# Optimization experiments

Measured on AMD Instinct MI355X. Metric: run time of the kernel, lower is better.

The kernel has to match this reference:

```python
import jax, jax.numpy as jnp
import numpy as np

BETA = 0.25

def setup_inputs() -> dict:
    key = jax.random.key(0)
    k1, k2 = jax.random.split(key)
    N, K, D = 262144, 1024, 64
    z = jax.random.normal(k1, (N, D), dtype=jnp.float32)
    codebook = jax.random.normal(k2, (K, D), dtype=jnp.float32)
    return {"z": z, "codebook": codebook}

def reference(z, codebook):
    # Squared Euclidean distances (argmin identical to torch.cdist argmin):
    # ||z||^2 - 2 z.C^T + ||C||^2 , shape [N, K]
    z_sq = jnp.sum(z * z, axis=1, keepdims=True)            # [N,1]
    c_sq = jnp.sum(codebook * codebook, axis=1)             # [K]
    dist = z_sq - 2.0 * (z @ codebook.T) + c_sq[None, :]    # [N,K]
    indices = jnp.argmin(dist, axis=1)                      # [N] int
    z_q = codebook[indices]                                 # [N,D]
    codebook_loss = jnp.mean((jax.lax.stop_gradient(z_q) - z) ** 2)
    commitment_loss = jnp.mean((z_q - jax.lax.stop_gradient(z)) ** 2)
    vq_loss = codebook_loss + BETA * commitment_loss
    z_q_st = z + jax.lax.stop_gradient(z_q - z)             # straight-through
    return (z_q_st, vq_loss, indices, z_q)
```

## Files before the change

kernel.cpp:

```cpp
#include <hip/hip_runtime.h>
#include <hip/hip_bf16.h>

typedef __bf16 bf16x8 __attribute__((ext_vector_type(8)));
typedef float  f32x4  __attribute__((ext_vector_type(4)));

static constexpr int N_ROWS  = 262144;
static constexpr int K_CODES = 1024;
static constexpr int D_DIM   = 64;

static constexpr long LOSS_OFF = (long)N_ROWS * D_DIM;
static constexpr long IDX_OFF  = LOSS_OFF + 1;
static constexpr long ZQ_OFF   = IDX_OFF + N_ROWS;

static constexpr size_t CSQ_B   = 0;
static constexpr size_t BFRAG_B = 4096;
static constexpr size_t CNT_B   = BFRAG_B + (size_t)16 * 16384;
static constexpr size_t PART_B  = CNT_B + 256;
static constexpr size_t LIST_B  = PART_B + (size_t)16384 * 4;
static constexpr size_t WS_NEEDED = LIST_B + (size_t)N_ROWS * 4;

static constexpr float MARGIN = 0.05f;
static constexpr int   EPI_BLOCKS = (N_ROWS * D_DIM) / (256 * 4);
static constexpr int   RESCORE_BLOCKS = 2048;

#define GLOAD_LDS16(g, l) __builtin_amdgcn_global_load_lds( \
    (const __attribute__((address_space(1))) unsigned int*)(g), \
    (__attribute__((address_space(3))) unsigned int*)(l), 16, 0, 0)

__global__ __launch_bounds__(256) void fusedprep_kernel(const float* __restrict__ cb,
                                                        char* __restrict__ wsb) {
    const int t = blockIdx.x * 256 + threadIdx.x;
    if (t == 0) *(int*)(wsb + CNT_B) = 0;

    if (t < K_CODES) {
        const float4* row = reinterpret_cast<const float4*>(cb) + (size_t)t * (D_DIM / 4);
        float s = 0.f;
        #pragma unroll
        for (int j = 0; j < D_DIM / 4; ++j) {
            float4 v = row[j];
            s = fmaf(v.x, v.x, s); s = fmaf(v.y, v.y, s);
            s = fmaf(v.z, v.z, s); s = fmaf(v.w, v.w, s);
        }
        ((float*)(wsb + CSQ_B))[t] = s;
    }

    const int c  = t >> 3;
    const int ks = (t >> 2) & 1;
    const int g  = t & 3;
    const float* src = cb + (size_t)c * 64 + ks * 32 + g * 8;
    float f[8];
    #pragma unroll
    for (int i = 0; i < 8; ++i) f[i] = src[i];
    bf16x8 h, l;
    #pragma unroll
    for (int i = 0; i < 8; ++i) {
        __bf16 hv = (__bf16)f[i];
        h[i] = hv;
        l[i] = (__bf16)(f[i] - (float)hv);
    }
    const int tile = c >> 6, cf = (c >> 4) & 3, n = c & 15;
    const int lane = g * 16 + n;
    char* base = wsb + BFRAG_B + (size_t)tile * 16384;
    *reinterpret_cast<bf16x8*>(base + ((0 * 2 + ks) * 4 + cf) * 1024 + lane * 16) = h;
    *reinterpret_cast<bf16x8*>(base + ((1 * 2 + ks) * 4 + cf) * 1024 + lane * 16) = l;
}

__global__ __launch_bounds__(256, 2) void vq_gemm_kernel(const float* __restrict__ z,
                                                         char* __restrict__ wsb,
                                                         float* __restrict__ out) {
    __shared__ __align__(16) unsigned char sbuf[2 * 16384 + 4096];
    float* lds_csq = (float*)(sbuf + 32768);

    const int tid  = threadIdx.x;
    const int lane = tid & 63, wid = tid >> 6;
    const int l15  = lane & 15, lg = lane >> 4;

    const float* csq = (const float*)(wsb + CSQ_B);
    #pragma unroll
    for (int i = 0; i < 4; ++i) lds_csq[tid + 256 * i] = csq[tid + 256 * i];

    const int rowbase = blockIdx.x * 256 + wid * 64;
    bf16x8 ah[4][2], al[4][2];
    #pragma unroll
    for (int rf = 0; rf < 4; ++rf) {
        const float* zr = z + (size_t)(rowbase + rf * 16 + l15) * 64 + lg * 8;
        #pragma unroll
        for (int ks = 0; ks < 2; ++ks) {
            float4 a = *reinterpret_cast<const float4*>(zr + ks * 32);
            float4 b = *reinterpret_cast<const float4*>(zr + ks * 32 + 4);
            float f[8] = {a.x, a.y, a.z, a.w, b.x, b.y, b.z, b.w};
            bf16x8 h, l;
            #pragma unroll
            for (int i = 0; i < 8; ++i) {
                __bf16 hv = (__bf16)f[i];
                h[i] = hv;
                l[i] = (__bf16)(f[i] - (float)hv);
            }
            ah[rf][ks] = h; al[rf][ks] = l;
        }
    }

    float m1[16], m2[16]; int i1[16];
    #pragma unroll
    for (int s = 0; s < 16; ++s) { m1[s] = INFINITY; m2[s] = INFINITY; i1[s] = 0; }

    const char* bsrc = wsb + BFRAG_B;
    auto stage = [&](int buf, int t) {
        const char* src = bsrc + (size_t)t * 16384;
        #pragma unroll
        for (int it = 0; it < 4; ++it) {
            GLOAD_LDS16(src + it * 4096 + wid * 1024 + lane * 16,
                        sbuf + buf * 16384 + it * 4096 + wid * 1024);
        }
    };

    stage(0, 0);
    __syncthreads();

    for (int t = 0; t < 16; ++t) {
        if (t < 15) stage((t + 1) & 1, t + 1);
        const unsigned char* B = sbuf + (t & 1) * 16384;
        #pragma unroll
        for (int cf = 0; cf < 4; ++cf) {
            bf16x8 bh0 = *reinterpret_cast<const bf16x8*>(B + (0 * 4 + cf) * 1024 + lane * 16);
            bf16x8 bh1 = *reinterpret_cast<const bf16x8*>(B + (1 * 4 + cf) * 1024 + lane * 16);
            bf16x8 bl0 = *reinterpret_cast<const bf16x8*>(B + (2 * 4 + cf) * 1024 + lane * 16);
            bf16x8 bl1 = *reinterpret_cast<const bf16x8*>(B + (3 * 4 + cf) * 1024 + lane * 16);
            const int code = t * 64 + cf * 16 + l15;
            const float cq = lds_csq[code];
            #pragma unroll
            for (int rf = 0; rf < 4; ++rf) {
                f32x4 acc = {0.f, 0.f, 0.f, 0.f};
                acc = __builtin_amdgcn_mfma_f32_16x16x32_bf16(ah[rf][0], bh0, acc, 0, 0, 0);
                acc = __builtin_amdgcn_mfma_f32_16x16x32_bf16(ah[rf][1], bh1, acc, 0, 0, 0);
                acc = __builtin_amdgcn_mfma_f32_16x16x32_bf16(al[rf][0], bh0, acc, 0, 0, 0);
                acc = __builtin_amdgcn_mfma_f32_16x16x32_bf16(al[rf][1], bh1, acc, 0, 0, 0);
                acc = __builtin_amdgcn_mfma_f32_16x16x32_bf16(ah[rf][0], bl0, acc, 0, 0, 0);
                acc = __builtin_amdgcn_mfma_f32_16x16x32_bf16(ah[rf][1], bl1, acc, 0, 0, 0);
                #pragma unroll
                for (int r = 0; r < 4; ++r) {
                    float dist = fmaf(-2.f, acc[r], cq);
                    int s = rf * 4 + r;
                    bool lt = dist < m1[s];
                    m2[s] = fminf(m2[s], fmaxf(dist, m1[s]));
                    m1[s] = fminf(m1[s], dist);
                    i1[s] = lt ? code : i1[s];
                }
            }
        }
        __syncthreads();
    }

    #pragma unroll
    for (int s = 0; s < 16; ++s) {
        #pragma unroll
        for (int off = 1; off < 16; off <<= 1) {
            float om1 = __shfl_xor(m1[s], off);
            float om2 = __shfl_xor(m2[s], off);
            int   oi  = __shfl_xor(i1[s], off);
            bool lt = (om1 < m1[s]) || (om1 == m1[s] && oi < i1[s]);
            m2[s] = fminf(fminf(m2[s], om2), fmaxf(m1[s], om1));
            m1[s] = fminf(m1[s], om1);
            i1[s] = lt ? oi : i1[s];
        }
    }

    if (l15 == 0) {
        int* cnt  = (int*)(wsb + CNT_B);
        int* list = (int*)(wsb + LIST_B);
        #pragma unroll
        for (int rf = 0; rf < 4; ++rf) {
            #pragma unroll
            for (int r = 0; r < 4; ++r) {
                int s = rf * 4 + r;
                int row = rowbase + rf * 16 + lg * 4 + r;
                out[IDX_OFF + row] = (float)i1[s];
                if (m2[s] - m1[s] < MARGIN) {
                    int pos = atomicAdd(cnt, 1);
                    if (pos < N_ROWS) list[pos] = row;
                }
            }
        }
    }
}

__global__ __launch_bounds__(256) void rescore_kernel(const float* __restrict__ z,
                                                      const float* __restrict__ cb,
                                                      const char* __restrict__ wsb,
                                                      float* __restrict__ out) {
    const int lane = threadIdx.x & 63;
    const int wgid = (blockIdx.x * 256 + threadIdx.x) >> 6;
    int cnt = *(const int*)(wsb + CNT_B);
    if (cnt > N_ROWS) cnt = N_ROWS;
    const int*   list = (const int*)(wsb + LIST_B);
    const float* csq  = (const float*)(wsb + CSQ_B);

    for (int i = wgid; i < cnt; i += RESCORE_BLOCKS * 4) {
        const int row = list[i];
        float4 zr[16];
        const float4* zp = reinterpret_cast<const float4*>(z) + (size_t)row * 16;
        #pragma unroll
        for (int j = 0; j < 16; ++j) zr[j] = zp[j];
        float best = INFINITY; int bi = 0;
        for (int k = lane; k < K_CODES; k += 64) {
            const float4* cp = reinterpret_cast<const float4*>(cb) + (size_t)k * 16;
            float d0 = 0.f, d1 = 0.f, d2 = 0.f, d3 = 0.f;
            #pragma unroll
            for (int j = 0; j < 16; j += 4) {
                float4 c0 = cp[j + 0], c1 = cp[j + 1], c2 = cp[j + 2], c3 = cp[j + 3];
                d0 = fmaf(zr[j+0].x, c0.x, fmaf(zr[j+0].y, c0.y, fmaf(zr[j+0].z, c0.z, fmaf(zr[j+0].w, c0.w, d0))));
                d1 = fmaf(zr[j+1].x, c1.x, fmaf(zr[j+1].y, c1.y, fmaf(zr[j+1].z, c1.z, fmaf(zr[j+1].w, c1.w, d1))));
                d2 = fmaf(zr[j+2].x, c2.x, fmaf(zr[j+2].y, c2.y, fmaf(zr[j+2].z, c2.z, fmaf(zr[j+2].w, c2.w, d2))));
                d3 = fmaf(zr[j+3].x, c3.x, fmaf(zr[j+3].y, c3.y, fmaf(zr[j+3].z, c3.z, fmaf(zr[j+3].w, c3.w, d3))));
            }
            float dist = fmaf(-2.f, (d0 + d1) + (d2 + d3), csq[k]);
            if (dist < best) { best = dist; bi = k; }
        }
        #pragma unroll
        for (int off = 1; off < 64; off <<= 1) {
            float ob = __shfl_xor(best, off);
            int   oi = __shfl_xor(bi, off);
            if (ob < best || (ob == best && oi < bi)) { best = ob; bi = oi; }
        }
        if (lane == 0) out[IDX_OFF + row] = (float)bi;
    }
}

__global__ __launch_bounds__(256) void gather_kernel(const float* __restrict__ z,
                                                     const float* __restrict__ cb,
                                                     float* __restrict__ out,
                                                     float* __restrict__ part) {
    const long g4 = (long)blockIdx.x * 256 + threadIdx.x;
    const long g  = g4 * 4;
    const int  r  = (int)(g >> 6);
    const int  d  = (int)(g & 63);
    const int k = (int)out[IDX_OFF + r];
    float4 zv = reinterpret_cast<const float4*>(z)[g4];
    float4 cv = reinterpret_cast<const float4*>(cb)[(long)k * 16 + (d >> 2)];
    float4 st;
    st.x = zv.x + (cv.x - zv.x); st.y = zv.y + (cv.y - zv.y);
    st.z = zv.z + (cv.z - zv.z); st.w = zv.w + (cv.w - zv.w);
    reinterpret_cast<float4*>(out)[g4] = st;
    float* zq = out + ZQ_OFF + g;
    zq[0] = cv.x; zq[1] = cv.y; zq[2] = cv.z; zq[3] = cv.w;
    float dx = cv.x - zv.x, dy = cv.y - zv.y, dz = cv.z - zv.z, dw = cv.w - zv.w;
    float s = fmaf(dx, dx, fmaf(dy, dy, fmaf(dz, dz, dw * dw)));
    #pragma unroll
    for (int off = 32; off > 0; off >>= 1) s += __shfl_down(s, off, 64);
    __shared__ float wsum[4];
    const int lane = threadIdx.x & 63, wid = threadIdx.x >> 6;
    if (lane == 0) wsum[wid] = s;
    __syncthreads();
    if (threadIdx.x == 0)
        part[blockIdx.x] = (wsum[0] + wsum[1]) + (wsum[2] + wsum[3]);
}

__global__ __launch_bounds__(256) void loss_kernel(const float* __restrict__ part,
                                                   float* __restrict__ out) {
    double s = 0.0;
    for (int i = threadIdx.x; i < EPI_BLOCKS; i += 256) s += (double)part[i];
    #pragma unroll
    for (int off = 32; off > 0; off >>= 1) s += __shfl_down(s, off, 64);
    __shared__ double dsum[4];
    const int lane = threadIdx.x & 63, wid = threadIdx.x >> 6;
    if (lane == 0) dsum[wid] = s;
    __syncthreads();
    if (threadIdx.x == 0) {
        double total = (dsum[0] + dsum[1]) + (dsum[2] + dsum[3]);
        out[LOSS_OFF] = (float)(1.25 * (total / (double)((long)N_ROWS * D_DIM)));
    }
}

__global__ __launch_bounds__(256) void csq_kernel(const float* __restrict__ cb,
                                                  float* __restrict__ ws) {
    int g = blockIdx.x * 256 + threadIdx.x;
    const float4* row = reinterpret_cast<const float4*>(cb) + (size_t)g * (D_DIM / 4);
    float s = 0.f;
    #pragma unroll
    for (int j = 0; j < D_DIM / 4; ++j) {
        float4 v = row[j];
        s = fmaf(v.x, v.x, s); s = fmaf(v.y, v.y, s);
        s = fmaf(v.z, v.z, s); s = fmaf(v.w, v.w, s);
    }
    ws[g] = s;
}

__global__ __launch_bounds__(256) void argmin_old_kernel(const float* __restrict__ z,
                                                         const float* __restrict__ cb,
                                                         const float* __restrict__ ws,
                                                         float* __restrict__ out) {
    __shared__ float4 tile[64 * 16];
    __shared__ float  csq_sh[64];
    const int row = blockIdx.x * 256 + threadIdx.x;
    float4 zr[16];
    const float4* zp = reinterpret_cast<const float4*>(z) + (size_t)row * 16;
    #pragma unroll
    for (int j = 0; j < 16; ++j) zr[j] = zp[j];
    float best = __builtin_inff();
    int   bidx = 0;
    for (int k0 = 0; k0 < K_CODES; k0 += 64) {
        __syncthreads();
        const float4* src = reinterpret_cast<const float4*>(cb) + (size_t)k0 * 16;
        #pragma unroll
        for (int j = 0; j < 4; ++j)
            tile[threadIdx.x + 256 * j] = src[threadIdx.x + 256 * j];
        if (threadIdx.x < 64) csq_sh[threadIdx.x] = ws[k0 + threadIdx.x];
        __syncthreads();
        #pragma unroll 2
        for (int k = 0; k < 64; ++k) {
            float d0 = 0.f, d1 = 0.f, d2 = 0.f, d3 = 0.f;
            #pragma unroll
            for (int j = 0; j < 16; j += 4) {
                float4 c0 = tile[k*16+j+0], c1 = tile[k*16+j+1], c2 = tile[k*16+j+2], c3 = tile[k*16+j+3];
                d0 = fmaf(zr[j+0].x, c0.x, fmaf(zr[j+0].y, c0.y, fmaf(zr[j+0].z, c0.z, fmaf(zr[j+0].w, c0.w, d0))));
                d1 = fmaf(zr[j+1].x, c1.x, fmaf(zr[j+1].y, c1.y, fmaf(zr[j+1].z, c1.z, fmaf(zr[j+1].w, c1.w, d1))));
                d2 = fmaf(zr[j+2].x, c2.x, fmaf(zr[j+2].y, c2.y, fmaf(zr[j+2].z, c2.z, fmaf(zr[j+2].w, c2.w, d2))));
                d3 = fmaf(zr[j+3].x, c3.x, fmaf(zr[j+3].y, c3.y, fmaf(zr[j+3].z, c3.z, fmaf(zr[j+3].w, c3.w, d3))));
            }
            float dist = fmaf(-2.f, (d0 + d1) + (d2 + d3), csq_sh[k]);
            if (dist < best) { best = dist; bidx = k0 + k; }
        }
    }
    out[IDX_OFF + row] = (float)bidx;
}

extern "C" void kernel_launch(void* const* d_in, const int* in_sizes, int n_in,
                              void* d_out, int out_size, void* d_ws, size_t ws_size,
                              hipStream_t stream) {
    (void)in_sizes; (void)n_in; (void)out_size;
    const float* z  = (const float*)d_in[0];
    const float* cb = (const float*)d_in[1];
    float* out = (float*)d_out;
    char*  wsb = (char*)d_ws;
    float* wsf = (float*)d_ws;

    if (ws_size >= WS_NEEDED) {
        fusedprep_kernel<<<32,             256, 0, stream>>>(cb, wsb);
        vq_gemm_kernel  <<<N_ROWS / 256,   256, 0, stream>>>(z, wsb, out);
        rescore_kernel  <<<RESCORE_BLOCKS, 256, 0, stream>>>(z, cb, wsb, out);
        gather_kernel   <<<EPI_BLOCKS,     256, 0, stream>>>(z, cb, out, (float*)(wsb + PART_B));
        loss_kernel     <<<1,              256, 0, stream>>>((const float*)(wsb + PART_B), out);
    } else {
        csq_kernel       <<<K_CODES / 256, 256, 0, stream>>>(cb, wsf);
        argmin_old_kernel<<<N_ROWS / 256,  256, 0, stream>>>(z, cb, wsf, out);
        gather_kernel    <<<EPI_BLOCKS,    256, 0, stream>>>(z, cb, out, wsf + 1024);
        loss_kernel      <<<1,             256, 0, stream>>>(wsf + 1024, out);
    }
}
```

Before: 396.0 us.

## Fold -2 scale and csq into MFMA accumulator; restructure rescore with LDS-tiled codebook

Prescales the codebook by -2 during bf16 split and seeds the MFMA accumulator with ||c||^2, removing one FMA per distance in the main GEMM loop. It also replaces the fmax/fmin second-best update with a single med3. The rescore kernel switches from one wavefront per row to one thread per row, with four waves each scanning a quarter of the codebook. Codebook tiles are staged in LDS and the per-wave minima are combined through shared memory. This reduces redundant global codebook reads per ambiguous row, but it adds block-wide syncs and lowers the rescore grid size.

```diff
diff --git a/kernel.cpp b/kernel.cpp
--- a/kernel.cpp
+++ b/kernel.cpp
@@ -21,7 +21,7 @@
 
 static constexpr float MARGIN = 0.05f;
 static constexpr int   EPI_BLOCKS = (N_ROWS * D_DIM) / (256 * 4);
-static constexpr int   RESCORE_BLOCKS = 2048;
+static constexpr int   RESCORE_BLOCKS = 512;
 
 #define GLOAD_LDS16(g, l) __builtin_amdgcn_global_load_lds( \
     (const __attribute__((address_space(1))) unsigned int*)(g), \
@@ -50,7 +50,7 @@
     const float* src = cb + (size_t)c * 64 + ks * 32 + g * 8;
     float f[8];
     #pragma unroll
-    for (int i = 0; i < 8; ++i) f[i] = src[i];
+    for (int i = 0; i < 8; ++i) f[i] = -2.0f * src[i];
     bf16x8 h, l;
     #pragma unroll
     for (int i = 0; i < 8; ++i) {
@@ -130,7 +130,7 @@
             const float cq = lds_csq[code];
             #pragma unroll
             for (int rf = 0; rf < 4; ++rf) {
-                f32x4 acc = {0.f, 0.f, 0.f, 0.f};
+                f32x4 acc = {cq, cq, cq, cq};
                 acc = __builtin_amdgcn_mfma_f32_16x16x32_bf16(ah[rf][0], bh0, acc, 0, 0, 0);
                 acc = __builtin_amdgcn_mfma_f32_16x16x32_bf16(ah[rf][1], bh1, acc, 0, 0, 0);
                 acc = __builtin_amdgcn_mfma_f32_16x16x32_bf16(al[rf][0], bh0, acc, 0, 0, 0);
@@ -139,10 +139,10 @@
                 acc = __builtin_amdgcn_mfma_f32_16x16x32_bf16(ah[rf][1], bl1, acc, 0, 0, 0);
                 #pragma unroll
                 for (int r = 0; r < 4; ++r) {
-                    float dist = fmaf(-2.f, acc[r], cq);
+                    float dist = acc[r];
                     int s = rf * 4 + r;
                     bool lt = dist < m1[s];
-                    m2[s] = fminf(m2[s], fmaxf(dist, m1[s]));
+                    m2[s] = __builtin_amdgcn_fmed3f(dist, m1[s], m2[s]);
                     m1[s] = fminf(m1[s], dist);
                     i1[s] = lt ? code : i1[s];
                 }
@@ -188,41 +188,75 @@
                                                       const float* __restrict__ cb,
                                                       const char* __restrict__ wsb,
                                                       float* __restrict__ out) {
-    const int lane = threadIdx.x & 63;
-    const int wgid = (blockIdx.x * 256 + threadIdx.x) >> 6;
+    __shared__ float4 tile[4][64 * 16];
+    __shared__ float  csq_sh[4][64];
+    __shared__ float  mbest[4][64];
+    __shared__ int    midx[4][64];
+
     int cnt = *(const int*)(wsb + CNT_B);
     if (cnt > N_ROWS) cnt = N_ROWS;
+    if (cnt == 0) return;
     const int*   list = (const int*)(wsb + LIST_B);
     const float* csq  = (const float*)(wsb + CSQ_B);
 
-    for (int i = wgid; i < cnt; i += RESCORE_BLOCKS * 4) {
-        const int row = list[i];
+    const int t    = threadIdx.x;
+    const int rloc = t & 63;
+    const int q    = t >> 6;
+
+    for (long i0 = (long)blockIdx.x * 64; i0 < cnt; i0 += (long)RESCORE_BLOCKS * 64) {
+        const long i = i0 + rloc;
+        const bool active = (i < cnt);
+        const int  row = list[active ? i : (cnt - 1)];
+
         float4 zr[16];
         const float4* zp = reinterpret_cast<const float4*>(z) + (size_t)row * 16;
         #pragma unroll
         for (int j = 0; j < 16; ++j) zr[j] = zp[j];
+
         float best = INFINITY; int bi = 0;
-        for (int k = lane; k < K_CODES; k += 64) {
-            const float4* cp = reinterpret_cast<const float4*>(cb) + (size_t)k * 16;
-            float d0 = 0.f, d1 = 0.f, d2 = 0.f, d3 = 0.f;
-            #pragma unroll
-            for (int j = 0; j < 16; j += 4) {
-                float4 c0 = cp[j + 0], c1 = cp[j + 1], c2 = cp[j + 2], c3 = cp[j + 3];
-                d0 = fmaf(zr[j+0].x, c0.x, fmaf(zr[j+0].y, c0.y, fmaf(zr[j+0].z, c0.z, fmaf(zr[j+0].w, c0.w, d0))));
-                d1 = fmaf(zr[j+1].x, c1.x, fmaf(zr[j+1].y, c1.y, fmaf(zr[j+1].z, c1.z, fmaf(zr[j+1].w, c1.w, d1))));
-                d2 = fmaf(zr[j+2].x, c2.x, fmaf(zr[j+2].y, c2.y, fmaf(zr[j+2].z, c2.z, fmaf(zr[j+2].w, c2.w, d2))));
-                d3 = fmaf(zr[j+3].x, c3.x, fmaf(zr[j+3].y, c3.y, fmaf(zr[j+3].z, c3.z, fmaf(zr[j+3].w, c3.w, d3))));
-            }
-            float dist = fmaf(-2.f, (d0 + d1) + (d2 + d3), csq[k]);
-            if (dist < best) { best = dist; bi = k; }
-        }
-        #pragma unroll
-        for (int off = 1; off < 64; off <<= 1) {
-            float ob = __shfl_xor(best, off);
-            int   oi = __shfl_xor(bi, off);
-            if (ob < best || (ob == best && oi < bi)) { best = ob; bi = oi; }
-        }
-        if (lane == 0) out[IDX_OFF + row] = (float)bi;
+
+        #pragma unroll 1
+        for (int j = 0; j < 4; ++j) {
+            __syncthreads();
+            #pragma unroll
+            for (int s = 0; s < 4; ++s) {
+                const float4* src = reinterpret_cast<const float4*>(cb) + (size_t)(s * 4 + j) * 64 * 16;
+                #pragma unroll
+                for (int u = 0; u < 4; ++u)
+                    tile[s][t + 256 * u] = src[t + 256 * u];
+            }
+            csq_sh[q][rloc] = csq[(q * 4 + j) * 64 + rloc];
+            __syncthreads();
+
+            const float4* T = tile[q];
+            const int cbase = (q * 4 + j) * 64;
+            #pragma unroll 2
+            for (int k = 0; k < 64; ++k) {
+                float d0 = 0.f, d1 = 0.f, d2 = 0.f, d3 = 0.f;
+                #pragma unroll
+                for (int jj = 0; jj < 16; jj += 4) {
+                    float4 c0 = T[k*16+jj+0], c1 = T[k*16+jj+1], c2 = T[k*16+jj+2], c3 = T[k*16+jj+3];
+                    d0 = fmaf(zr[jj+0].x, c0.x, fmaf(zr[jj+0].y, c0.y, fmaf(zr[jj+0].z, c0.z, fmaf(zr[jj+0].w, c0.w, d0))));
+                    d1 = fmaf(zr[jj+1].x, c1.x, fmaf(zr[jj+1].y, c1.y, fmaf(zr[jj+1].z, c1.z, fmaf(zr[jj+1].w, c1.w, d1))));
+                    d2 = fmaf(zr[jj+2].x, c2.x, fmaf(zr[jj+2].y, c2.y, fmaf(zr[jj+2].z, c2.z, fmaf(zr[jj+2].w, c2.w, d2))));
+                    d3 = fmaf(zr[jj+3].x, c3.x, fmaf(zr[jj+3].y, c3.y, fmaf(zr[jj+3].z, c3.z, fmaf(zr[jj+3].w, c3.w, d3))));
+                }
+                float dist = fmaf(-2.f, (d0 + d1) + (d2 + d3), csq_sh[q][k]);
+                if (dist < best) { best = dist; bi = cbase + k; }
+            }
+        }
+
+        mbest[q][rloc] = best; midx[q][rloc] = bi;
+        __syncthreads();
+        if (q == 0 && active) {
+            float b = mbest[0][rloc]; int x = midx[0][rloc];
+            #pragma unroll
+            for (int s = 1; s < 4; ++s) {
+                float ob = mbest[s][rloc]; int ox = midx[s][rloc];
+                if (ob < b || (ob == b && ox < x)) { b = ob; x = ox; }
+            }
+            out[IDX_OFF + row] = (float)x;
+        }
     }
 }
 
```

Measured after the change: 395.5 us. Within noise of the previous version (-0.1%).
